# Kernel optimization log

Hardware: AMD Instinct MI355X
Metric: run time of the kernel (lower is better)

## Reference

```python
import jax, jax.numpy as jnp
import numpy as np

EMBED_DIM = 768
NUM_HEADS = 12
HEAD_DIM = EMBED_DIM // NUM_HEADS
B, S = 2, 2048


def setup_inputs() -> dict:
    key = jax.random.key(0)
    k1, k2, k3, k4, k5 = jax.random.split(key, 5)
    scale = 1.0 / np.sqrt(EMBED_DIM)
    return {
        "x": jax.random.normal(k1, (B, S, EMBED_DIM), dtype=jnp.float32),
        "w_qkv": jax.random.normal(k2, (EMBED_DIM, 3 * EMBED_DIM), dtype=jnp.float32) * scale,
        "b_qkv": jax.random.normal(k3, (3 * EMBED_DIM,), dtype=jnp.float32) * 0.01,
        "w_proj": jax.random.normal(k4, (EMBED_DIM, EMBED_DIM), dtype=jnp.float32) * scale,
        "b_proj": jax.random.normal(k5, (EMBED_DIM,), dtype=jnp.float32) * 0.01,
    }


def reference(x, w_qkv, b_qkv, w_proj, b_proj):
    b, s, e = x.shape
    h, d = NUM_HEADS, HEAD_DIM
    # fused QKV projection: [b, s, 3, h, d]
    qkv = (x @ w_qkv + b_qkv).reshape(b, s, 3, h, d)
    q = qkv[:, :, 0].transpose(0, 2, 1, 3)  # [b, h, s, d]
    k = qkv[:, :, 1].transpose(0, 2, 1, 3)
    v = qkv[:, :, 2].transpose(0, 2, 1, 3)
    scores = jnp.einsum("bhqd,bhkd->bhqk", q, k) * (d ** -0.5)
    attn = jax.nn.softmax(scores, axis=-1)  # dropout is identity in eval mode
    out = jnp.einsum("bhqk,bhkd->bhqd", attn, v)
    out = out.transpose(0, 2, 1, 3).reshape(b, s, e)
    return out @ w_proj + b_proj
```

## Files before the change

### kernel.cpp

```cpp
#include <hip/hip_runtime.h>
#include <hip/hip_bf16.h>


typedef __bf16 bf16x8 __attribute__((ext_vector_type(8)));
typedef float f32x4 __attribute__((ext_vector_type(4)));
typedef unsigned short ushortx8 __attribute__((ext_vector_type(8)));
typedef unsigned short ushortx4 __attribute__((ext_vector_type(4)));

#define EMB 768
#define SEQ 2048
#define NBATCH 2
#define NHEAD 12
#define HDIM 64
#define MROWS (NBATCH*SEQ)
#define NQKV (3*EMB)

static __device__ __forceinline__ unsigned short b16(float f) {
  __hip_bfloat16 h = __float2bfloat16(f);
  return __builtin_bit_cast(unsigned short, h);
}

static __device__ __forceinline__ void gld16(const void* g, void* l) {
  __builtin_amdgcn_global_load_lds((const __attribute__((address_space(1))) void*)g,
                                   (__attribute__((address_space(3))) void*)l, 16, 0, 0);
}

__global__ __launch_bounds__(256) void k_cvt_bf16(const float* __restrict__ in,
                                                  unsigned short* __restrict__ out, int n) {
  int i = (blockIdx.x * 256 + threadIdx.x) * 4;
  if (i >= n) return;
  f32x4 v = *(const f32x4*)(in + i);
  ushortx4 o;
  o[0] = b16(v[0]); o[1] = b16(v[1]); o[2] = b16(v[2]); o[3] = b16(v[3]);
  *(ushortx4*)(out + i) = o;
}

__global__ __launch_bounds__(256) void k_tcvt(const float* __restrict__ in,
                                              unsigned short* __restrict__ out,
                                              int K, int N) {
  __shared__ float t[64][65];
  const int n0 = blockIdx.x * 64, k0 = blockIdx.y * 64;
  const int x = threadIdx.x & 63, y0 = threadIdx.x >> 6;
  #pragma unroll
  for (int i = 0; i < 16; ++i) {
    int r = y0 * 16 + i;
    t[r][x] = in[(size_t)(k0 + r) * N + n0 + x];
  }
  __syncthreads();
  #pragma unroll
  for (int i = 0; i < 16; ++i) {
    int r = y0 * 16 + i;
    out[(size_t)(n0 + r) * K + k0 + x] = b16(t[x][r]);
  }
}

static __device__ __forceinline__ void gemm_tile_128(
    const unsigned short* __restrict__ A, const unsigned short* __restrict__ B,
    int K, int bm, int bn, unsigned short* Alds, unsigned short* Blds, f32x4 acc[4][4]) {
  const int tid = threadIdx.x;
  const int lane = tid & 63, w = tid >> 6;
  const int l15 = lane & 15, lg = lane >> 4;
  const int wm = w >> 1, wn = w & 1;
  #pragma unroll
  for (int m = 0; m < 4; ++m)
    #pragma unroll
    for (int n = 0; n < 4; ++n)
      acc[m][n] = (f32x4){0.f, 0.f, 0.f, 0.f};

  const size_t aoff1 = (size_t)(bm * 128 + (tid >> 2)) * K + (tid & 3) * 8;
  const size_t aoff2 = (size_t)(bm * 128 + (tid >> 2) + 64) * K + (tid & 3) * 8;
  const size_t boff1 = (size_t)(bn * 128 + (tid >> 2)) * K + (tid & 3) * 8;
  const size_t boff2 = (size_t)(bn * 128 + (tid >> 2) + 64) * K + (tid & 3) * 8;
  char* lA = (char*)Alds;
  char* lB = (char*)Blds;
  const char* aBase = (const char*)Alds + (wm * 64 + l15) * 64 + lg * 16;
  const char* bBase = (const char*)Blds + (wn * 64 + l15) * 64 + lg * 16;

  gld16(A + aoff1, lA + w * 1024);
  gld16(A + aoff2, lA + 4096 + w * 1024);
  gld16(B + boff1, lB + w * 1024);
  gld16(B + boff2, lB + 4096 + w * 1024);

  const int T = K >> 5;
  for (int t = 0; t < T; ++t) {
    const int cur = t & 1;
    if (t + 1 < T) {
      const int k1 = (t + 1) << 5;
      char* ad = lA + (cur ^ 1) * 8192 + w * 1024;
      char* bd = lB + (cur ^ 1) * 8192 + w * 1024;
      gld16(A + aoff1 + k1, ad);
      gld16(A + aoff2 + k1, ad + 4096);
      gld16(B + boff1 + k1, bd);
      gld16(B + boff2 + k1, bd + 4096);
      asm volatile("s_waitcnt vmcnt(4)" ::: "memory");
    } else {
      asm volatile("s_waitcnt vmcnt(0)" ::: "memory");
    }
    __builtin_amdgcn_s_barrier();
    const char* ab = aBase + cur * 8192;
    const char* bb = bBase + cur * 8192;
    bf16x8 af[4], bfr[4];
    #pragma unroll
    for (int m = 0; m < 4; ++m) af[m] = *(const bf16x8*)(ab + m * 1024);
    #pragma unroll
    for (int n = 0; n < 4; ++n) bfr[n] = *(const bf16x8*)(bb + n * 1024);
    #pragma unroll
    for (int m = 0; m < 4; ++m)
      #pragma unroll
      for (int n = 0; n < 4; ++n)
        acc[m][n] = __builtin_amdgcn_mfma_f32_16x16x32_bf16(af[m], bfr[n], acc[m][n], 0, 0, 0);
    if (t + 1 < T) __builtin_amdgcn_s_barrier();
  }
}

#define QSCALE 0.18033688011112042f
__global__ __launch_bounds__(256) void k_gemm_qkv(
    const unsigned short* __restrict__ Xb, const unsigned short* __restrict__ Wt,
    const float* __restrict__ bias,
    unsigned short* __restrict__ Qb, unsigned short* __restrict__ Kb,
    unsigned short* __restrict__ VTb) {
  __shared__ __align__(16) unsigned short Alds[2 * 128 * 32];
  __shared__ __align__(16) unsigned short Blds[2 * 128 * 32];
  f32x4 acc[4][4];
  const int bm = blockIdx.x, bn = blockIdx.y;
  gemm_tile_128(Xb, Wt, EMB, bm, bn, Alds, Blds, acc);
  const int tid = threadIdx.x, lane = tid & 63, w = tid >> 6;
  const int l15 = lane & 15, lg = lane >> 4, wm = w >> 1, wn = w & 1;
  #pragma unroll
  for (int m = 0; m < 4; ++m)
    #pragma unroll
    for (int n = 0; n < 4; ++n)
      #pragma unroll
      for (int r = 0; r < 4; ++r) {
        int gr = bm * 128 + wm * 64 + m * 16 + lg * 4 + r;
        int gc = bn * 128 + wn * 64 + n * 16 + l15;
        float v = acc[m][n][r] + bias[gc];
        int t = gc / 768, rem = gc % 768;
        int h = rem >> 6, d = rem & 63;
        int b = gr >> 11, s = gr & 2047;
        int bh = b * 12 + h;
        if (t == 0)      Qb[((size_t)bh * 2048 + s) * 64 + d] = b16(v * QSCALE);
        else if (t == 1) Kb[((size_t)bh * 2048 + s) * 64 + d] = b16(v);
        else {
          int sp = (s & ~0x1C) | ((s & 0x0C) << 1) | ((s & 0x10) >> 2);
          VTb[((size_t)bh * 64 + d) * 2048 + sp] = b16(v);
        }
      }
}

__global__ __launch_bounds__(256) void k_gemm_proj(
    const unsigned short* __restrict__ Ab, const unsigned short* __restrict__ Wt,
    const float* __restrict__ bias, float* __restrict__ out) {
  __shared__ __align__(16) unsigned short Alds[2 * 128 * 32];
  __shared__ __align__(16) unsigned short Blds[2 * 128 * 32];
  f32x4 acc[4][4];
  const int bm = blockIdx.x, bn = blockIdx.y;
  gemm_tile_128(Ab, Wt, EMB, bm, bn, Alds, Blds, acc);
  const int tid = threadIdx.x, lane = tid & 63, w = tid >> 6;
  const int l15 = lane & 15, lg = lane >> 4, wm = w >> 1, wn = w & 1;
  #pragma unroll
  for (int m = 0; m < 4; ++m)
    #pragma unroll
    for (int n = 0; n < 4; ++n)
      #pragma unroll
      for (int r = 0; r < 4; ++r) {
        int gr = bm * 128 + wm * 64 + m * 16 + lg * 4 + r;
        int gc = bn * 128 + wn * 64 + n * 16 + l15;
        out[(size_t)gr * EMB + gc] = acc[m][n][r] + bias[gc];
      }
}

__global__ __launch_bounds__(256) void k_attn(
    const unsigned short* __restrict__ Qg, const unsigned short* __restrict__ Kg,
    const unsigned short* __restrict__ VTg, unsigned short* __restrict__ AO) {
  __shared__ __align__(16) char KL[2 * 8192];
  __shared__ __align__(16) char VTL[2 * 8192];
  const int bid = blockIdx.x;
  const int bh = bid >> 5, qt = bid & 31;
  const int b = bh / 12, h = bh % 12;
  const size_t base = (size_t)bh * (SEQ * HDIM);
  const int tid = threadIdx.x, lane = tid & 63, w = tid >> 6;
  const int l15 = lane & 15, lg = lane >> 4;
  const int swz = (l15 & 7) << 4;

  bf16x8 qf[2];
  {
    const size_t qoff = base + (size_t)(qt * 64 + w * 16 + l15) * 64 + lg * 8;
    qf[0] = *(const bf16x8*)(Qg + qoff);
    qf[1] = *(const bf16x8*)(Qg + qoff + 32);
  }

  const int srow0 = tid >> 3;
  const int scg0 = (tid & 7) ^ (srow0 & 7);
  const int scg1 = (tid & 7) ^ ((srow0 + 32) & 7);

  f32x4 Oacc[4];
  #pragma unroll
  for (int nd = 0; nd < 4; ++nd) Oacc[nd] = (f32x4){0.f, 0.f, 0.f, 0.f};
  float l_ = 0.f;

  gld16(Kg + base + (size_t)srow0 * 64 + scg0 * 8,            KL + w * 1024);
  gld16(Kg + base + (size_t)(srow0 + 32) * 64 + scg1 * 8,     KL + 4096 + w * 1024);
  gld16(VTg + base + (size_t)srow0 * 2048 + scg0 * 8,         VTL + w * 1024);
  gld16(VTg + base + (size_t)(srow0 + 32) * 2048 + scg1 * 8,  VTL + 4096 + w * 1024);
  __syncthreads();

  for (int t = 0; t < 32; ++t) {
    const int bi = t & 1;
    if (t < 31) {
      const int kv1 = (t + 1) * 64;
      char* kd = KL + (bi ^ 1) * 8192 + w * 1024;
      char* vd = VTL + (bi ^ 1) * 8192 + w * 1024;
      gld16(Kg + base + (size_t)(kv1 + srow0) * 64 + scg0 * 8,           kd);
      gld16(Kg + base + (size_t)(kv1 + srow0 + 32) * 64 + scg1 * 8,      kd + 4096);
      gld16(VTg + base + (size_t)srow0 * 2048 + kv1 + scg0 * 8,          vd);
      gld16(VTg + base + (size_t)(srow0 + 32) * 2048 + kv1 + scg1 * 8,   vd + 4096);
    }
    const char* kb = KL + bi * 8192;
    const char* vb = VTL + bi * 8192;

    f32x4 sv[4];
    __builtin_amdgcn_s_setprio(1);
    #pragma unroll
    for (int n = 0; n < 4; ++n) {
      const char* rb = kb + (n * 16 + l15) * 128;
      bf16x8 kf0 = *(const bf16x8*)(rb + ((lg * 16) ^ swz));
      bf16x8 kf1 = *(const bf16x8*)(rb + ((64 + lg * 16) ^ swz));
      f32x4 z = (f32x4){0.f, 0.f, 0.f, 0.f};
      z = __builtin_amdgcn_mfma_f32_16x16x32_bf16(kf0, qf[0], z, 0, 0, 0);
      sv[n] = __builtin_amdgcn_mfma_f32_16x16x32_bf16(kf1, qf[1], z, 0, 0, 0);
    }

    #pragma unroll
    for (int c = 0; c < 2; ++c) {
      ushortx8 up;
      #pragma unroll
      for (int j = 0; j < 4; ++j) {
        float pa = __builtin_amdgcn_exp2f(sv[2 * c][j]);
        float pb = __builtin_amdgcn_exp2f(sv[2 * c + 1][j]);
        l_ += pa + pb;
        up[j] = b16(pa);
        up[4 + j] = b16(pb);
      }
      bf16x8 pfB = __builtin_bit_cast(bf16x8, up);
      #pragma unroll
      for (int nd = 0; nd < 4; ++nd) {
        const char* vr = vb + (nd * 16 + l15) * 128;
        bf16x8 vf = *(const bf16x8*)(vr + ((c * 64 + lg * 16) ^ swz));
        Oacc[nd] = __builtin_amdgcn_mfma_f32_16x16x32_bf16(vf, pfB, Oacc[nd], 0, 0, 0);
      }
    }
    __builtin_amdgcn_s_setprio(0);
    __syncthreads();
  }

  l_ += __shfl_xor(l_, 16);
  l_ += __shfl_xor(l_, 32);
  const float rl = 1.0f / l_;
  const int q = qt * 64 + w * 16 + l15;
  #pragma unroll
  for (int nd = 0; nd < 4; ++nd) {
    ushortx4 o;
    #pragma unroll
    for (int r = 0; r < 4; ++r) o[r] = b16(Oacc[nd][r] * rl);
    *(ushortx4*)(AO + ((size_t)(b * 2048 + q)) * EMB + h * 64 + nd * 16 + lg * 4) = o;
  }
}

extern "C" void kernel_launch(void* const* d_in, const int* in_sizes, int n_in,
                              void* d_out, int out_size, void* d_ws, size_t ws_size,
                              hipStream_t stream) {
  const float* x     = (const float*)d_in[0];
  const float* wqkv  = (const float*)d_in[1];
  const float* bqkv  = (const float*)d_in[2];
  const float* wproj = (const float*)d_in[3];
  const float* bproj = (const float*)d_in[4];
  float* out = (float*)d_out;
  char* ws = (char*)d_ws;

  unsigned short* xb     = (unsigned short*)(ws + 0);
  unsigned short* wqkvT  = (unsigned short*)(ws + 6291456);
  unsigned short* wprojT = (unsigned short*)(ws + 9830400);
  unsigned short* Qb     = (unsigned short*)(ws + 11010048);
  unsigned short* Kb     = (unsigned short*)(ws + 17301504);
  unsigned short* VTb    = (unsigned short*)(ws + 23592960);
  unsigned short* AOb    = (unsigned short*)(ws + 29884416);

  k_cvt_bf16<<<3072, 256, 0, stream>>>(x, xb, MROWS * EMB);
  k_tcvt<<<dim3(NQKV / 64, EMB / 64), 256, 0, stream>>>(wqkv, wqkvT, EMB, NQKV);
  k_tcvt<<<dim3(EMB / 64, EMB / 64), 256, 0, stream>>>(wproj, wprojT, EMB, EMB);
  k_gemm_qkv<<<dim3(MROWS / 128, NQKV / 128), 256, 0, stream>>>(xb, wqkvT, bqkv, Qb, Kb, VTb);
  k_attn<<<24 * (SEQ / 64), 256, 0, stream>>>(Qb, Kb, VTb, AOb);
  k_gemm_proj<<<dim3(MROWS / 128, EMB / 128), 256, 0, stream>>>(AOb, wprojT, bproj, out);
}
```

Measured before the change: 99.24 us.

## Merge prep kernels, deepen GEMM K-tile, give attention warps two Q tiles

Three conversion/transpose kernels are merged into one launch to cut launch overhead. The shared GEMM tile now stages K=64 per step with XOR-swizzled LDS rows, halving the barrier count per K. The attention kernel drops to 128 threads, with each warp handling two 16-row Q tiles so every K/V fragment read from LDS feeds twice as many MFMAs. It also computes the softmax denominator with an MFMA against a ones vector instead of scalar adds and shuffles. The cost is more registers per thread and fewer warps per block in attention.

```diff
diff --git a/kernel.cpp b/kernel.cpp
--- a/kernel.cpp
+++ b/kernel.cpp
@@ -9,11 +9,11 @@
 
 #define EMB 768
 #define SEQ 2048
-#define NBATCH 2
 #define NHEAD 12
 #define HDIM 64
-#define MROWS (NBATCH*SEQ)
-#define NQKV (3*EMB)
+#define MROWS 4096
+#define NQKV 2304
+#define QSCALE 0.18033688011112042f
 
 static __device__ __forceinline__ unsigned short b16(float f) {
   __hip_bfloat16 h = __float2bfloat16(f);
@@ -25,40 +25,36 @@
                                    (__attribute__((address_space(3))) void*)l, 16, 0, 0);
 }
 
-__global__ __launch_bounds__(256) void k_cvt_bf16(const float* __restrict__ in,
-                                                  unsigned short* __restrict__ out, int n) {
-  int i = (blockIdx.x * 256 + threadIdx.x) * 4;
-  if (i >= n) return;
-  f32x4 v = *(const f32x4*)(in + i);
-  ushortx4 o;
-  o[0] = b16(v[0]); o[1] = b16(v[1]); o[2] = b16(v[2]); o[3] = b16(v[3]);
-  *(ushortx4*)(out + i) = o;
-}
-
-__global__ __launch_bounds__(256) void k_tcvt(const float* __restrict__ in,
-                                              unsigned short* __restrict__ out,
-                                              int K, int N) {
+__global__ __launch_bounds__(256) void k_prep(
+    const float* __restrict__ x, const float* __restrict__ wqkv, const float* __restrict__ wproj,
+    unsigned short* __restrict__ xb, unsigned short* __restrict__ wqkvT,
+    unsigned short* __restrict__ wprojT) {
   __shared__ float t[64][65];
-  const int n0 = blockIdx.x * 64, k0 = blockIdx.y * 64;
-  const int x = threadIdx.x & 63, y0 = threadIdx.x >> 6;
-  #pragma unroll
-  for (int i = 0; i < 16; ++i) {
-    int r = y0 * 16 + i;
-    t[r][x] = in[(size_t)(k0 + r) * N + n0 + x];
-  }
+  const int bid = blockIdx.x;
+  if (bid < 3072) {
+    int i = (bid * 256 + threadIdx.x) * 4;
+    f32x4 v = *(const f32x4*)(x + i);
+    ushortx4 o;
+    o[0] = b16(v[0]); o[1] = b16(v[1]); o[2] = b16(v[2]); o[3] = b16(v[3]);
+    *(ushortx4*)(xb + i) = o;
+    return;
+  }
+  const float* in; unsigned short* out; int N, bx, by;
+  if (bid < 3072 + 432) { in = wqkv;  out = wqkvT;  N = NQKV; int r = bid - 3072; bx = r % 36; by = r / 36; }
+  else                  { in = wproj; out = wprojT; N = EMB;  int r = bid - 3504; bx = r % 12; by = r / 12; }
+  const int n0 = bx * 64, k0 = by * 64;
+  const int xx = threadIdx.x & 63, y0 = threadIdx.x >> 6;
+  #pragma unroll
+  for (int i = 0; i < 16; ++i) { int r = y0 * 16 + i; t[r][xx] = in[(size_t)(k0 + r) * N + n0 + xx]; }
   __syncthreads();
   #pragma unroll
-  for (int i = 0; i < 16; ++i) {
-    int r = y0 * 16 + i;
-    out[(size_t)(n0 + r) * K + k0 + x] = b16(t[x][r]);
-  }
+  for (int i = 0; i < 16; ++i) { int r = y0 * 16 + i; out[(size_t)(n0 + r) * EMB + k0 + xx] = b16(t[xx][r]); }
 }
 
 static __device__ __forceinline__ void gemm_tile_128(
     const unsigned short* __restrict__ A, const unsigned short* __restrict__ B,
-    int K, int bm, int bn, unsigned short* Alds, unsigned short* Blds, f32x4 acc[4][4]) {
-  const int tid = threadIdx.x;
-  const int lane = tid & 63, w = tid >> 6;
+    int K, int bm, int bn, char* lA, char* lB, f32x4 acc[4][4]) {
+  const int tid = threadIdx.x, lane = tid & 63, w = tid >> 6;
   const int l15 = lane & 15, lg = lane >> 4;
   const int wm = w >> 1, wn = w & 1;
   #pragma unroll
@@ -67,60 +63,69 @@
     for (int n = 0; n < 4; ++n)
       acc[m][n] = (f32x4){0.f, 0.f, 0.f, 0.f};
 
-  const size_t aoff1 = (size_t)(bm * 128 + (tid >> 2)) * K + (tid & 3) * 8;
-  const size_t aoff2 = (size_t)(bm * 128 + (tid >> 2) + 64) * K + (tid & 3) * 8;
-  const size_t boff1 = (size_t)(bn * 128 + (tid >> 2)) * K + (tid & 3) * 8;
-  const size_t boff2 = (size_t)(bn * 128 + (tid >> 2) + 64) * K + (tid & 3) * 8;
-  char* lA = (char*)Alds;
-  char* lB = (char*)Blds;
-  const char* aBase = (const char*)Alds + (wm * 64 + l15) * 64 + lg * 16;
-  const char* bBase = (const char*)Blds + (wn * 64 + l15) * 64 + lg * 16;
-
-  gld16(A + aoff1, lA + w * 1024);
-  gld16(A + aoff2, lA + 4096 + w * 1024);
-  gld16(B + boff1, lB + w * 1024);
-  gld16(B + boff2, lB + 4096 + w * 1024);
-
-  const int T = K >> 5;
+  const int srow = w * 32 + (lane >> 3);
+  const int glog = (lane & 7) ^ (lane >> 3);
+  const size_t abase = (size_t)(bm * 128 + srow) * K + glog * 8;
+  const size_t bbase = (size_t)(bn * 128 + srow) * K + glog * 8;
+  const char* aB = lA + (wm * 64 + l15) * 128;
+  const char* bB = lB + (wn * 64 + l15) * 128;
+  const int rsw = (l15 & 7) << 4;
+
+  const int T = K >> 6;
+  {
+    char* ad = lA + w * 4096; char* bd = lB + w * 4096;
+    #pragma unroll
+    for (int j = 0; j < 4; ++j) {
+      gld16(A + abase + (size_t)j * 8 * K, ad + j * 1024);
+      gld16(B + bbase + (size_t)j * 8 * K, bd + j * 1024);
+    }
+  }
   for (int t = 0; t < T; ++t) {
     const int cur = t & 1;
     if (t + 1 < T) {
-      const int k1 = (t + 1) << 5;
-      char* ad = lA + (cur ^ 1) * 8192 + w * 1024;
-      char* bd = lB + (cur ^ 1) * 8192 + w * 1024;
-      gld16(A + aoff1 + k1, ad);
-      gld16(A + aoff2 + k1, ad + 4096);
-      gld16(B + boff1 + k1, bd);
-      gld16(B + boff2 + k1, bd + 4096);
-      asm volatile("s_waitcnt vmcnt(4)" ::: "memory");
+      const int k1 = (t + 1) << 6;
+      char* ad = lA + (cur ^ 1) * 16384 + w * 4096;
+      char* bd = lB + (cur ^ 1) * 16384 + w * 4096;
+      #pragma unroll
+      for (int j = 0; j < 4; ++j) {
+        gld16(A + abase + (size_t)j * 8 * K + k1, ad + j * 1024);
+        gld16(B + bbase + (size_t)j * 8 * K + k1, bd + j * 1024);
+      }
+      asm volatile("s_waitcnt vmcnt(8)" ::: "memory");
     } else {
       asm volatile("s_waitcnt vmcnt(0)" ::: "memory");
     }
     __builtin_amdgcn_s_barrier();
-    const char* ab = aBase + cur * 8192;
-    const char* bb = bBase + cur * 8192;
-    bf16x8 af[4], bfr[4];
-    #pragma unroll
-    for (int m = 0; m < 4; ++m) af[m] = *(const bf16x8*)(ab + m * 1024);
-    #pragma unroll
-    for (int n = 0; n < 4; ++n) bfr[n] = *(const bf16x8*)(bb + n * 1024);
-    #pragma unroll
-    for (int m = 0; m < 4; ++m)
+    const char* ab = aB + cur * 16384;
+    const char* bb = bB + cur * 16384;
+    bf16x8 af[2][4], bfr[2][4];
+    #pragma unroll
+    for (int kk = 0; kk < 2; ++kk) {
+      #pragma unroll
+      for (int m = 0; m < 4; ++m)
+        af[kk][m] = *(const bf16x8*)(ab + m * 2048 + (((kk * 4 + lg) * 16) ^ rsw));
       #pragma unroll
       for (int n = 0; n < 4; ++n)
-        acc[m][n] = __builtin_amdgcn_mfma_f32_16x16x32_bf16(af[m], bfr[n], acc[m][n], 0, 0, 0);
+        bfr[kk][n] = *(const bf16x8*)(bb + n * 2048 + (((kk * 4 + lg) * 16) ^ rsw));
+    }
+    #pragma unroll
+    for (int kk = 0; kk < 2; ++kk)
+      #pragma unroll
+      for (int m = 0; m < 4; ++m)
+        #pragma unroll
+        for (int n = 0; n < 4; ++n)
+          acc[m][n] = __builtin_amdgcn_mfma_f32_16x16x32_bf16(af[kk][m], bfr[kk][n], acc[m][n], 0, 0, 0);
     if (t + 1 < T) __builtin_amdgcn_s_barrier();
   }
 }
 
-#define QSCALE 0.18033688011112042f
 __global__ __launch_bounds__(256) void k_gemm_qkv(
     const unsigned short* __restrict__ Xb, const unsigned short* __restrict__ Wt,
     const float* __restrict__ bias,
     unsigned short* __restrict__ Qb, unsigned short* __restrict__ Kb,
     unsigned short* __restrict__ VTb) {
-  __shared__ __align__(16) unsigned short Alds[2 * 128 * 32];
-  __shared__ __align__(16) unsigned short Blds[2 * 128 * 32];
+  __shared__ __align__(16) char Alds[2 * 16384];
+  __shared__ __align__(16) char Blds[2 * 16384];
   f32x4 acc[4][4];
   const int bm = blockIdx.x, bn = blockIdx.y;
   gemm_tile_128(Xb, Wt, EMB, bm, bn, Alds, Blds, acc);
@@ -151,8 +156,8 @@
 __global__ __launch_bounds__(256) void k_gemm_proj(
     const unsigned short* __restrict__ Ab, const unsigned short* __restrict__ Wt,
     const float* __restrict__ bias, float* __restrict__ out) {
-  __shared__ __align__(16) unsigned short Alds[2 * 128 * 32];
-  __shared__ __align__(16) unsigned short Blds[2 * 128 * 32];
+  __shared__ __align__(16) char Alds[2 * 16384];
+  __shared__ __align__(16) char Blds[2 * 16384];
   f32x4 acc[4][4];
   const int bm = blockIdx.x, bn = blockIdx.y;
   gemm_tile_128(Ab, Wt, EMB, bm, bn, Alds, Blds, acc);
@@ -170,7 +175,7 @@
       }
 }
 
-__global__ __launch_bounds__(256) void k_attn(
+__global__ __launch_bounds__(128) void k_attn(
     const unsigned short* __restrict__ Qg, const unsigned short* __restrict__ Kg,
     const unsigned short* __restrict__ VTg, unsigned short* __restrict__ AO) {
   __shared__ __align__(16) char KL[2 * 8192];
@@ -183,87 +188,112 @@
   const int l15 = lane & 15, lg = lane >> 4;
   const int swz = (l15 & 7) << 4;
 
-  bf16x8 qf[2];
+  bf16x8 qf0a, qf0b, qf1a, qf1b;
   {
-    const size_t qoff = base + (size_t)(qt * 64 + w * 16 + l15) * 64 + lg * 8;
-    qf[0] = *(const bf16x8*)(Qg + qoff);
-    qf[1] = *(const bf16x8*)(Qg + qoff + 32);
-  }
-
-  const int srow0 = tid >> 3;
-  const int scg0 = (tid & 7) ^ (srow0 & 7);
-  const int scg1 = (tid & 7) ^ ((srow0 + 32) & 7);
-
-  f32x4 Oacc[4];
-  #pragma unroll
-  for (int nd = 0; nd < 4; ++nd) Oacc[nd] = (f32x4){0.f, 0.f, 0.f, 0.f};
-  float l_ = 0.f;
-
-  gld16(Kg + base + (size_t)srow0 * 64 + scg0 * 8,            KL + w * 1024);
-  gld16(Kg + base + (size_t)(srow0 + 32) * 64 + scg1 * 8,     KL + 4096 + w * 1024);
-  gld16(VTg + base + (size_t)srow0 * 2048 + scg0 * 8,         VTL + w * 1024);
-  gld16(VTg + base + (size_t)(srow0 + 32) * 2048 + scg1 * 8,  VTL + 4096 + w * 1024);
+    const size_t qoff = base + (size_t)(qt * 64 + w * 32 + l15) * 64 + lg * 8;
+    qf0a = *(const bf16x8*)(Qg + qoff);
+    qf0b = *(const bf16x8*)(Qg + qoff + 32);
+    qf1a = *(const bf16x8*)(Qg + qoff + 16 * 64);
+    qf1b = *(const bf16x8*)(Qg + qoff + 16 * 64 + 32);
+  }
+
+  const int srow = w * 32 + (lane >> 3);
+  const int glog = (lane & 7) ^ (lane >> 3);
+
+  ushortx8 os;
+  #pragma unroll
+  for (int j = 0; j < 8; ++j) os[j] = 0x3F80;
+  const bf16x8 onesf = __builtin_bit_cast(bf16x8, os);
+
+  f32x4 Oacc0[4], Oacc1[4];
+  #pragma unroll
+  for (int nd = 0; nd < 4; ++nd) {
+    Oacc0[nd] = (f32x4){0.f, 0.f, 0.f, 0.f};
+    Oacc1[nd] = (f32x4){0.f, 0.f, 0.f, 0.f};
+  }
+  f32x4 Lacc0 = (f32x4){0.f, 0.f, 0.f, 0.f};
+  f32x4 Lacc1 = (f32x4){0.f, 0.f, 0.f, 0.f};
+
+  #pragma unroll
+  for (int j = 0; j < 4; ++j) {
+    gld16(Kg + base + (size_t)(srow + j * 8) * 64 + glog * 8,          KL + w * 4096 + j * 1024);
+    gld16(VTg + base + (size_t)(srow + j * 8) * 2048 + glog * 8,       VTL + w * 4096 + j * 1024);
+  }
   __syncthreads();
 
   for (int t = 0; t < 32; ++t) {
     const int bi = t & 1;
     if (t < 31) {
       const int kv1 = (t + 1) * 64;
-      char* kd = KL + (bi ^ 1) * 8192 + w * 1024;
-      char* vd = VTL + (bi ^ 1) * 8192 + w * 1024;
-      gld16(Kg + base + (size_t)(kv1 + srow0) * 64 + scg0 * 8,           kd);
-      gld16(Kg + base + (size_t)(kv1 + srow0 + 32) * 64 + scg1 * 8,      kd + 4096);
-      gld16(VTg + base + (size_t)srow0 * 2048 + kv1 + scg0 * 8,          vd);
-      gld16(VTg + base + (size_t)(srow0 + 32) * 2048 + kv1 + scg1 * 8,   vd + 4096);
+      char* kd = KL + (bi ^ 1) * 8192 + w * 4096;
+      char* vd = VTL + (bi ^ 1) * 8192 + w * 4096;
+      #pragma unroll
+      for (int j = 0; j < 4; ++j) {
+        gld16(Kg + base + (size_t)(kv1 + srow + j * 8) * 64 + glog * 8,    kd + j * 1024);
+        gld16(VTg + base + (size_t)(srow + j * 8) * 2048 + kv1 + glog * 8, vd + j * 1024);
+      }
     }
     const char* kb = KL + bi * 8192;
     const char* vb = VTL + bi * 8192;
 
-    f32x4 sv[4];
+    f32x4 sv0[4], sv1[4];
     __builtin_amdgcn_s_setprio(1);
     #pragma unroll
     for (int n = 0; n < 4; ++n) {
       const char* rb = kb + (n * 16 + l15) * 128;
       bf16x8 kf0 = *(const bf16x8*)(rb + ((lg * 16) ^ swz));
       bf16x8 kf1 = *(const bf16x8*)(rb + ((64 + lg * 16) ^ swz));
-      f32x4 z = (f32x4){0.f, 0.f, 0.f, 0.f};
-      z = __builtin_amdgcn_mfma_f32_16x16x32_bf16(kf0, qf[0], z, 0, 0, 0);
-      sv[n] = __builtin_amdgcn_mfma_f32_16x16x32_bf16(kf1, qf[1], z, 0, 0, 0);
-    }
-
+      f32x4 z0 = (f32x4){0.f, 0.f, 0.f, 0.f};
+      z0 = __builtin_amdgcn_mfma_f32_16x16x32_bf16(kf0, qf0a, z0, 0, 0, 0);
+      sv0[n] = __builtin_amdgcn_mfma_f32_16x16x32_bf16(kf1, qf0b, z0, 0, 0, 0);
+      f32x4 z1 = (f32x4){0.f, 0.f, 0.f, 0.f};
+      z1 = __builtin_amdgcn_mfma_f32_16x16x32_bf16(kf0, qf1a, z1, 0, 0, 0);
+      sv1[n] = __builtin_amdgcn_mfma_f32_16x16x32_bf16(kf1, qf1b, z1, 0, 0, 0);
+    }
+
+    bf16x8 pf0[2], pf1[2];
     #pragma unroll
     for (int c = 0; c < 2; ++c) {
-      ushortx8 up;
+      ushortx8 u0, u1;
       #pragma unroll
       for (int j = 0; j < 4; ++j) {
-        float pa = __builtin_amdgcn_exp2f(sv[2 * c][j]);
-        float pb = __builtin_amdgcn_exp2f(sv[2 * c + 1][j]);
-        l_ += pa + pb;
-        up[j] = b16(pa);
-        up[4 + j] = b16(pb);
-      }
-      bf16x8 pfB = __builtin_bit_cast(bf16x8, up);
+        u0[j]     = b16(__builtin_amdgcn_exp2f(sv0[2 * c][j]));
+        u0[4 + j] = b16(__builtin_amdgcn_exp2f(sv0[2 * c + 1][j]));
+        u1[j]     = b16(__builtin_amdgcn_exp2f(sv1[2 * c][j]));
+        u1[4 + j] = b16(__builtin_amdgcn_exp2f(sv1[2 * c + 1][j]));
+      }
+      pf0[c] = __builtin_bit_cast(bf16x8, u0);
+      pf1[c] = __builtin_bit_cast(bf16x8, u1);
+      Lacc0 = __builtin_amdgcn_mfma_f32_16x16x32_bf16(onesf, pf0[c], Lacc0, 0, 0, 0);
+      Lacc1 = __builtin_amdgcn_mfma_f32_16x16x32_bf16(onesf, pf1[c], Lacc1, 0, 0, 0);
+    }
+
+    #pragma unroll
+    for (int c = 0; c < 2; ++c) {
       #pragma unroll
       for (int nd = 0; nd < 4; ++nd) {
-        const char* vr = vb + (nd * 16 + l15) * 128;
-        bf16x8 vf = *(const bf16x8*)(vr + ((c * 64 + lg * 16) ^ swz));
-        Oacc[nd] = __builtin_amdgcn_mfma_f32_16x16x32_bf16(vf, pfB, Oacc[nd], 0, 0, 0);
+        bf16x8 vf = *(const bf16x8*)(vb + (nd * 16 + l15) * 128 + ((c * 64 + lg * 16) ^ swz));
+        Oacc0[nd] = __builtin_amdgcn_mfma_f32_16x16x32_bf16(vf, pf0[c], Oacc0[nd], 0, 0, 0);
+        Oacc1[nd] = __builtin_amdgcn_mfma_f32_16x16x32_bf16(vf, pf1[c], Oacc1[nd], 0, 0, 0);
       }
     }
     __builtin_amdgcn_s_setprio(0);
     __syncthreads();
   }
 
-  l_ += __shfl_xor(l_, 16);
-  l_ += __shfl_xor(l_, 32);
-  const float rl = 1.0f / l_;
-  const int q = qt * 64 + w * 16 + l15;
+  const int q0 = qt * 64 + w * 32 + l15;
+  const float rl0 = 1.0f / Lacc0[0];
+  const float rl1 = 1.0f / Lacc1[0];
   #pragma unroll
   for (int nd = 0; nd < 4; ++nd) {
-    ushortx4 o;
-    #pragma unroll
-    for (int r = 0; r < 4; ++r) o[r] = b16(Oacc[nd][r] * rl);
-    *(ushortx4*)(AO + ((size_t)(b * 2048 + q)) * EMB + h * 64 + nd * 16 + lg * 4) = o;
+    ushortx4 o0, o1;
+    #pragma unroll
+    for (int r = 0; r < 4; ++r) {
+      o0[r] = b16(Oacc0[nd][r] * rl0);
+      o1[r] = b16(Oacc1[nd][r] * rl1);
+    }
+    *(ushortx4*)(AO + ((size_t)(b * 2048 + q0)) * EMB + h * 64 + nd * 16 + lg * 4) = o0;
+    *(ushortx4*)(AO + ((size_t)(b * 2048 + q0 + 16)) * EMB + h * 64 + nd * 16 + lg * 4) = o1;
   }
 }
 
@@ -286,10 +316,8 @@
   unsigned short* VTb    = (unsigned short*)(ws + 23592960);
   unsigned short* AOb    = (unsigned short*)(ws + 29884416);
 
-  k_cvt_bf16<<<3072, 256, 0, stream>>>(x, xb, MROWS * EMB);
-  k_tcvt<<<dim3(NQKV / 64, EMB / 64), 256, 0, stream>>>(wqkv, wqkvT, EMB, NQKV);
-  k_tcvt<<<dim3(EMB / 64, EMB / 64), 256, 0, stream>>>(wproj, wprojT, EMB, EMB);
+  k_prep<<<3648, 256, 0, stream>>>(x, wqkv, wproj, xb, wqkvT, wprojT);
   k_gemm_qkv<<<dim3(MROWS / 128, NQKV / 128), 256, 0, stream>>>(xb, wqkvT, bqkv, Qb, Kb, VTb);
-  k_attn<<<24 * (SEQ / 64), 256, 0, stream>>>(Qb, Kb, VTb, AOb);
+  k_attn<<<24 * (SEQ / 64), 128, 0, stream>>>(Qb, Kb, VTb, AOb);
   k_gemm_proj<<<dim3(MROWS / 128, EMB / 128), 256, 0, stream>>>(AOb, wprojT, bproj, out);
 }
```

Result: slower. 112.8 us (+13.7%).
